# Kernel tuning notes

Measured on AMD Instinct MI355X. Metric: run time of the kernel, lower is better.

The kernel has to match this reference:

```python
import jax, jax.numpy as jnp
import numpy as np

N = 8192        # nodes (A.shape[0])
D_IN = 128      # input_dim
D_OUT = 128     # output_dim
D_THETA = 256   # hardcoded in GCN_liner_theta_1
DROP_KEEP = 0.8 # DropEdge percent


def setup_inputs() -> dict:
    key = jax.random.key(0)
    ks = jax.random.split(key, 6)
    H = jax.random.normal(ks[0], (N, D_IN), dtype=jnp.float32)
    U = jax.random.uniform(ks[1], (N, N), dtype=jnp.float32)
    upper = jnp.triu((U < 0.01).astype(jnp.float32), 1)
    A_adj = upper + upper.T + jnp.eye(N, dtype=jnp.float32)
    bn_gamma = jnp.ones((D_IN,), jnp.float32)
    bn_beta = jnp.zeros((D_IN,), jnp.float32)
    W_theta = jax.random.normal(ks[2], (D_THETA, D_IN), jnp.float32) * 0.05
    b_theta = jnp.zeros((D_THETA,), jnp.float32)
    W_out = jax.random.normal(ks[3], (D_OUT, D_IN), jnp.float32) * 0.05
    b_out = jnp.zeros((D_OUT,), jnp.float32)
    return {"H": H, "A_adj": A_adj, "bn_gamma": bn_gamma, "bn_beta": bn_beta,
            "W_theta": W_theta, "b_theta": b_theta, "W_out": W_out, "b_out": b_out}


def reference(H, A_adj, bn_gamma, bn_beta, W_theta, b_theta, W_out, b_out):
    n = H.shape[0]
    # BatchNorm1d in training mode: batch stats over the node dimension
    mean = H.mean(axis=0)
    var = H.var(axis=0)  # biased, matches torch training normalization
    Hn = (H - mean) * jax.lax.rsqrt(var + 1e-5) * bn_gamma + bn_beta

    # theta projection -> pairwise euclidean distances
    Hx = Hn @ W_theta.T + b_theta                     # [N, 256]
    sq = jnp.sum(Hx * Hx, axis=1)                     # [N]
    dist = sq[:, None] + sq[None, :] - 2.0 * (Hx @ Hx.T)
    dist = jnp.sqrt(jnp.clip(dist, 1e-12, None))      # [N, N]

    A = jnp.exp(-0.2 * dist)
    A = jnp.clip(jax.nn.sigmoid(A), 0.1, None)
    # DropEdge detaches A in the original (A never carries grad)
    A = jax.lax.stop_gradient(A)

    dkey = jax.random.key(42)
    keep = jax.random.uniform(dkey, (n, n)) < DROP_KEEP
    triu = jnp.triu(jnp.ones((n, n), dtype=bool), 0)
    Bt = jnp.where(triu & keep, A, 0.0)
    B = Bt + Bt.T - jnp.diag(jnp.diag(Bt))

    mask = jnp.ceil(A_adj * 1e-5)
    A2 = B * mask + jnp.eye(n, dtype=B.dtype)
    A3 = jnp.where(A2 > 0.6, A2, 0.0)                 # threshold (host loop in torch)

    # symmetric normalization D^-1/2 A D^-1/2 without dense diag matmuls
    d_inv_sqrt = jax.lax.rsqrt(A3.sum(axis=1))        # diag always >= 1
    A_hat = A3 * d_inv_sqrt[:, None] * d_inv_sqrt[None, :]

    out = A_hat @ (Hn @ W_out.T + b_out)              # [N, D_OUT]
    out = jnp.where(out >= 0, out, 0.01 * out)        # LeakyReLU(0.01)
    return out, A3
```

## Files before the change

### kernel.cpp

```cpp
#include <hip/hip_runtime.h>
#include <cstdint>
#include <cstddef>

#define N 8192
#define DIN 128
#define DTH 256
#define DOUT 128
#define ROWCAP 256
#define LISTCAP 256

typedef float vfloat4 __attribute__((ext_vector_type(4)));

__device__ __forceinline__ void threefry_0_42(uint32_t x0, uint32_t x1,
                                              uint32_t& o0, uint32_t& o1) {
  const uint32_t ks0 = 0u;
  const uint32_t ks1 = 42u;
  const uint32_t ks2 = 0x1BD11BDAu ^ 0u ^ 42u;
  x0 += ks0; x1 += ks1;
#define TF_R(r) { x0 += x1; x1 = (x1 << (r)) | (x1 >> (32 - (r))); x1 ^= x0; }
  TF_R(13) TF_R(15) TF_R(26) TF_R(6)
  x0 += ks1; x1 += ks2 + 1u;
  TF_R(17) TF_R(29) TF_R(16) TF_R(24)
  x0 += ks2; x1 += ks0 + 2u;
  TF_R(13) TF_R(15) TF_R(26) TF_R(6)
  x0 += ks0; x1 += ks1 + 3u;
  TF_R(17) TF_R(29) TF_R(16) TF_R(24)
  x0 += ks1; x1 += ks2 + 4u;
  TF_R(13) TF_R(15) TF_R(26) TF_R(6)
  x0 += ks2; x1 += ks0 + 5u;
#undef TF_R
  o0 = x0; o1 = x1;
}

__device__ __forceinline__ bool dropedge_keep(uint32_t t) {
  uint32_t y0, y1;
  threefry_0_42(0u, t, y0, y1);
  uint32_t bits = y0 ^ y1;
  float u = __uint_as_float((bits >> 9) | 0x3f800000u) - 1.0f;
  return u < 0.8f;
}

__device__ __forceinline__ unsigned short f2bf(float v) {
  uint32_t u = __float_as_uint(v);
  u += 0x7fffu + ((u >> 16) & 1u);
  return (unsigned short)(u >> 16);
}

__global__ __launch_bounds__(256) void k_pre(
    const float* __restrict__ H,
    const float* __restrict__ Wt, const float* __restrict__ bt,
    const float* __restrict__ Wo, const float* __restrict__ bo,
    float* __restrict__ part_s, float* __restrict__ part_s2,
    float* __restrict__ Wc, float* __restrict__ bc,
    float* __restrict__ deg ) {
  int b = blockIdx.x;
  int tid = threadIdx.x;
  if (b < 64) {
    __shared__ float ls[8][DIN];
    __shared__ float ls2[8][DIN];
    int rg = tid >> 5;
    int c4 = tid & 31;
    int rbase = b * 128;
    float s[4] = {0,0,0,0}, s2[4] = {0,0,0,0};
    for (int k = 0; k < 16; ++k) {
      int r = rbase + rg + k * 8;
      float4 h = ((const float4*)(H + (size_t)r * DIN))[c4];
      s[0] += h.x; s2[0] += h.x * h.x;
      s[1] += h.y; s2[1] += h.y * h.y;
      s[2] += h.z; s2[2] += h.z * h.z;
      s[3] += h.w; s2[3] += h.w * h.w;
    }
#pragma unroll
    for (int q = 0; q < 4; ++q) { ls[rg][c4*4+q] = s[q]; ls2[rg][c4*4+q] = s2[q]; }
    __syncthreads();
    if (tid < DIN) {
      float a = 0.f, bb = 0.f;
#pragma unroll
      for (int g = 0; g < 8; ++g) { a += ls[g][tid]; bb += ls2[g][tid]; }
      part_s[b * DIN + tid] = a;
      part_s2[b * DIN + tid] = bb;
    }
  } else if (b < 256) {
    int idx = (b - 64) * 256 + tid;
    int k = idx / 384, c = idx % 384;
    Wc[idx] = (c < 256) ? Wt[(size_t)c * DIN + k] : Wo[(size_t)(c - 256) * DIN + k];
  } else if (b < 258) {
    int c = (b - 256) * 256 + tid;
    if (c < 384) bc[c] = (c < 256) ? bt[c] : bo[c - 256];
  } else {
    int g = (b - 258) * 256 + tid;
    ((int4*)deg)[g] = make_int4(0, 0, 0, 0);
  }
}

__global__ __launch_bounds__(256) void k_rows(
    const float* __restrict__ H,
    const float* __restrict__ part_s, const float* __restrict__ part_s2,
    const float* __restrict__ gamma, const float* __restrict__ beta,
    const float* __restrict__ Wc, const float* __restrict__ bc,
    unsigned short* __restrict__ Hxh, float* __restrict__ HW,
    float* __restrict__ sq, float* __restrict__ A3) {
  int tid = threadIdx.x;
  int b = blockIdx.x;
  if (b >= 512) {
    vfloat4* row = (vfloat4*)(A3 + (size_t)(b - 512) * N);
    const vfloat4 z = {0.f, 0.f, 0.f, 0.f};
#pragma unroll
    for (int it = 0; it < 8; ++it)
      __builtin_nontemporal_store(z, row + tid + it * 256);
    return;
  }
  __shared__ __align__(16) float ssc[DIN];
  __shared__ __align__(16) float ssh[DIN];
  __shared__ float hn[16][DIN];
  if (tid < DIN) {
    float s = 0.f, s2 = 0.f;
    for (int g = 0; g < 64; ++g) { s += part_s[g*DIN+tid]; s2 += part_s2[g*DIN+tid]; }
    float mean = s * (1.0f / N);
    float var  = s2 * (1.0f / N) - mean * mean;
    float sc = rsqrtf(var + 1e-5f) * gamma[tid];
    ssc[tid] = sc;
    ssh[tid] = beta[tid] - mean * sc;
  }
  __syncthreads();
  int base = b * 16;
#pragma unroll
  for (int k = 0; k < 2; ++k) {
    int f = tid + k * 256;
    int r = f >> 5, c4 = f & 31;
    float4 h  = ((const float4*)(H + (size_t)(base + r) * DIN))[c4];
    float4 sc = ((const float4*)ssc)[c4];
    float4 sh = ((const float4*)ssh)[c4];
    h.x = h.x * sc.x + sh.x; h.y = h.y * sc.y + sh.y;
    h.z = h.z * sc.z + sh.z; h.w = h.w * sc.w + sh.w;
    ((float4*)hn[r])[c4] = h;
  }
  __syncthreads();
  int w = tid >> 6, lane = tid & 63;
  int r0 = w * 4;
  float acc[4][6];
#pragma unroll
  for (int r = 0; r < 4; ++r)
#pragma unroll
    for (int q = 0; q < 6; ++q) acc[r][q] = 0.f;

  for (int k4 = 0; k4 < 32; ++k4) {
    float4 h[4];
#pragma unroll
    for (int r = 0; r < 4; ++r) h[r] = ((const float4*)hn[r0 + r])[k4];
#pragma unroll
    for (int kk = 0; kk < 4; ++kk) {
      const float* wrow = Wc + (size_t)(k4 * 4 + kk) * 384 + lane;
      float wv[6];
#pragma unroll
      for (int q = 0; q < 6; ++q) wv[q] = wrow[64 * q];
#pragma unroll
      for (int r = 0; r < 4; ++r) {
        float hs = (kk == 0) ? h[r].x : (kk == 1) ? h[r].y
                 : (kk == 2) ? h[r].z : h[r].w;
#pragma unroll
        for (int q = 0; q < 6; ++q) acc[r][q] += hs * wv[q];
      }
    }
  }
#pragma unroll
  for (int r = 0; r < 4; ++r) {
    int row = base + r0 + r;
    float s = 0.f;
#pragma unroll
    for (int q = 0; q < 4; ++q) {
      float v = acc[r][q] + bc[lane + 64 * q];
      Hxh[(size_t)row * DTH + lane + 64 * q] = f2bf(v);
      s += v * v;
    }
#pragma unroll
    for (int off = 32; off > 0; off >>= 1) s += __shfl_xor(s, off, 64);
    if (lane == 0) sq[row] = s;
#pragma unroll
    for (int q = 4; q < 6; ++q) {
      float v = acc[r][q] + bc[lane + 64 * q];
      HW[(size_t)row * DOUT + lane + 64 * (q - 4)] = v;
    }
  }
}

__global__ __launch_bounds__(256) void k_main(
    const float* __restrict__ A_adj, const unsigned short* __restrict__ Hxh,
    const float* __restrict__ sq, float* __restrict__ A3,
    float* __restrict__ deg, int* __restrict__ nnz_cnt,
    int* __restrict__ nnz_idx, float* __restrict__ nnz_val) {
  int i = blockIdx.x;
  int tid = threadIdx.x;
  __shared__ float4 hx4[64];
  __shared__ int   s_list[LISTCAP];
  __shared__ int   s_cnt;
  if (tid == 0) s_cnt = 0;
  ((float*)hx4)[tid] = __uint_as_float(((uint32_t)Hxh[(size_t)i * DTH + tid]) << 16);
  __syncthreads();

  const vfloat4* arow = (const vfloat4*)(A_adj + (size_t)i * N);
  int q0 = i >> 2;
  for (int q4 = q0 + tid; q4 < N / 4; q4 += 256) {
    vfloat4 a = __builtin_nontemporal_load(arow + q4);
    int jb = q4 * 4;
    float av[4] = {a.x, a.y, a.z, a.w};
#pragma unroll
    for (int q = 0; q < 4; ++q) {
      int j = jb + q;
      if (av[q] != 0.f && j >= i) {
        int p = atomicAdd(&s_cnt, 1);
        if (p < LISTCAP) s_list[p] = j;
      }
    }
  }
  __syncthreads();

  int M = min(s_cnt, LISTCAP);
  float sqi = sq[i];
  for (int t = tid; t < M; t += 256) {
    int j = s_list[t];
    bool keep = dropedge_keep((uint32_t)i * (uint32_t)N + (uint32_t)j);
    float dist;
    if (j == i) {
      dist = 1e-6f;
    } else {
      const uint4* hj = (const uint4*)(Hxh + (size_t)j * DTH);
      float dot = 0.f;
#pragma unroll 8
      for (int c = 0; c < 32; ++c) {
        uint4 u = hj[c];
        float4 f0 = hx4[2 * c], f1 = hx4[2 * c + 1];
        dot += __uint_as_float(u.x << 16) * f0.x
             + __uint_as_float(u.x & 0xffff0000u) * f0.y
             + __uint_as_float(u.y << 16) * f0.z
             + __uint_as_float(u.y & 0xffff0000u) * f0.w
             + __uint_as_float(u.z << 16) * f1.x
             + __uint_as_float(u.z & 0xffff0000u) * f1.y
             + __uint_as_float(u.w << 16) * f1.z
             + __uint_as_float(u.w & 0xffff0000u) * f1.w;
      }
      dist = sqrtf(fmaxf(sqi + sq[j] - 2.0f * dot, 1e-12f));
    }
    float aval = expf(-0.2f * dist);
    float sg = fmaxf(1.0f / (1.0f + expf(-aval)), 0.1f);
    float bb = keep ? sg : 0.0f;
    float a2 = bb + ((i == j) ? 1.0f : 0.0f);
    float a3v = (a2 > 0.6f) ? a2 : 0.0f;
    if (a3v != 0.f) {
      A3[(size_t)i * N + j] = a3v;
      atomicAdd(&deg[i], a3v);
      int p = atomicAdd(&nnz_cnt[i], 1);
      if (p < ROWCAP) {
        nnz_idx[(size_t)i * ROWCAP + p] = j;
        nnz_val[(size_t)i * ROWCAP + p] = a3v;
      }
      if (j != i) {
        A3[(size_t)j * N + i] = a3v;
        atomicAdd(&deg[j], a3v);
        int p2 = atomicAdd(&nnz_cnt[j], 1);
        if (p2 < ROWCAP) {
          nnz_idx[(size_t)j * ROWCAP + p2] = i;
          nnz_val[(size_t)j * ROWCAP + p2] = a3v;
        }
      }
    }
  }
}

__global__ __launch_bounds__(128) void k_post(
    const float* __restrict__ HW, const float* __restrict__ deg,
    const int* __restrict__ nnz_cnt, const int* __restrict__ nnz_idx,
    const float* __restrict__ nnz_val, float* __restrict__ out) {
  int i = blockIdx.x;
  int c = threadIdx.x;
  int cnt = min(nnz_cnt[i], ROWCAP);
  float acc = 0.f;
  for (int e = 0; e < cnt; ++e) {
    int j = nnz_idx[(size_t)i * ROWCAP + e];
    float v = nnz_val[(size_t)i * ROWCAP + e];
    acc += v * rsqrtf(deg[j]) * HW[(size_t)j * DOUT + c];
  }
  float o = rsqrtf(deg[i]) * acc;
  out[(size_t)i * DOUT + c] = (o >= 0.f) ? o : 0.01f * o;
}

extern "C" void kernel_launch(void* const* d_in, const int* in_sizes, int n_in,
                              void* d_out, int out_size, void* d_ws, size_t ws_size,
                              hipStream_t stream) {
  const float* H     = (const float*)d_in[0];
  const float* A_adj = (const float*)d_in[1];
  const float* gamma = (const float*)d_in[2];
  const float* beta  = (const float*)d_in[3];
  const float* Wt    = (const float*)d_in[4];
  const float* bt    = (const float*)d_in[5];
  const float* Wo    = (const float*)d_in[6];
  const float* bo    = (const float*)d_in[7];

  float* out = (float*)d_out;
  float* A3  = out + (size_t)N * DOUT;

  float* ws    = (float*)d_ws;
  unsigned short* Hxh = (unsigned short*)ws;
  float* sq    = ws + (size_t)N * 128;
  float* HW    = sq + N;
  float* deg   = HW + (size_t)N * DOUT;
  int*   nnz_cnt = (int*)(deg + N);
  int*   nnz_idx = nnz_cnt + N;
  float* nnz_val = (float*)(nnz_idx + (size_t)N * ROWCAP);
  float* part_s  = nnz_val + (size_t)N * ROWCAP;
  float* part_s2 = part_s + 64 * DIN;
  float* Wc      = part_s2 + 64 * DIN;
  float* bc      = Wc + 128 * 384;

  k_pre<<<274, 256, 0, stream>>>(H, Wt, bt, Wo, bo, part_s, part_s2, Wc, bc, deg);
  k_rows<<<512 + N, 256, 0, stream>>>(H, part_s, part_s2, gamma, beta, Wc, bc,
                                      Hxh, HW, sq, A3);
  k_main<<<N, 256, 0, stream>>>(A_adj, Hxh, sq, A3, deg, nnz_cnt, nnz_idx, nnz_val);
  k_post<<<N, DOUT, 0, stream>>>(HW, deg, nnz_cnt, nnz_idx, nnz_val, out);
}
```

Measured before the change: 461.4 us.

## Move adjacency scan into row-projection kernel and shrink edge kernel to one wavefront

The scan of the dense adjacency matrix that builds each row's upper-triangular edge list moves out of the edge kernel. It now runs in the same launch as the row projection and A3 zeroing, on extra blocks, and writes a compact 16-bit edge index list and count per row to workspace. The edge kernel then reads these lists and runs with 64 threads per row instead of 256. The aim is to overlap the bandwidth-bound adjacency read with the projection's compute and zero-fill, and to stop the low-parallelism edge work from occupying wide blocks. The cost is an extra global round-trip for the edge lists, and the 16-bit indices rely on N fitting in unsigned short.

Result: slower. 473.9 us (+2.7%).

```diff
diff --git a/kernel.cpp b/kernel.cpp
--- a/kernel.cpp
+++ b/kernel.cpp
@@ -93,21 +93,52 @@
   }
 }
 
-__global__ __launch_bounds__(256) void k_rows(
+__global__ __launch_bounds__(256) void k_mid(
     const float* __restrict__ H,
     const float* __restrict__ part_s, const float* __restrict__ part_s2,
     const float* __restrict__ gamma, const float* __restrict__ beta,
     const float* __restrict__ Wc, const float* __restrict__ bc,
+    const float* __restrict__ A_adj,
     unsigned short* __restrict__ Hxh, float* __restrict__ HW,
-    float* __restrict__ sq, float* __restrict__ A3) {
+    float* __restrict__ sq, float* __restrict__ A3,
+    unsigned short* __restrict__ edge_idx, int* __restrict__ edge_cnt) {
   int tid = threadIdx.x;
   int b = blockIdx.x;
   if (b >= 512) {
-    vfloat4* row = (vfloat4*)(A3 + (size_t)(b - 512) * N);
-    const vfloat4 z = {0.f, 0.f, 0.f, 0.f};
-#pragma unroll
-    for (int it = 0; it < 8; ++it)
-      __builtin_nontemporal_store(z, row + tid + it * 256);
+    int t = b - 512;
+    int row = t >> 1;
+    if ((t & 1) == 0) {
+      vfloat4* rp = (vfloat4*)(A3 + (size_t)row * N);
+      const vfloat4 z = {0.f, 0.f, 0.f, 0.f};
+#pragma unroll
+      for (int it = 0; it < 8; ++it)
+        __builtin_nontemporal_store(z, rp + tid + it * 256);
+    } else {
+      __shared__ unsigned short s_list[LISTCAP];
+      __shared__ int s_cnt;
+      if (tid == 0) s_cnt = 0;
+      __syncthreads();
+      const vfloat4* arow = (const vfloat4*)(A_adj + (size_t)row * N);
+      int q0 = row >> 2;
+      for (int q4 = q0 + tid; q4 < N / 4; q4 += 256) {
+        vfloat4 a = __builtin_nontemporal_load(arow + q4);
+        int jb = q4 * 4;
+        float av[4] = {a.x, a.y, a.z, a.w};
+#pragma unroll
+        for (int q = 0; q < 4; ++q) {
+          int j = jb + q;
+          if (av[q] != 0.f && j >= row) {
+            int p = atomicAdd(&s_cnt, 1);
+            if (p < LISTCAP) s_list[p] = (unsigned short)j;
+          }
+        }
+      }
+      __syncthreads();
+      int M = min(s_cnt, LISTCAP);
+      for (int t2 = tid; t2 < M; t2 += 256)
+        edge_idx[(size_t)row * LISTCAP + t2] = s_list[t2];
+      if (tid == 0) edge_cnt[row] = M;
+    }
     return;
   }
   __shared__ __align__(16) float ssc[DIN];
@@ -184,41 +215,21 @@
   }
 }
 
-__global__ __launch_bounds__(256) void k_main(
-    const float* __restrict__ A_adj, const unsigned short* __restrict__ Hxh,
-    const float* __restrict__ sq, float* __restrict__ A3,
-    float* __restrict__ deg, int* __restrict__ nnz_cnt,
+__global__ __launch_bounds__(64) void k_edges(
+    const unsigned short* __restrict__ Hxh, const float* __restrict__ sq,
+    const unsigned short* __restrict__ edge_idx, const int* __restrict__ edge_cnt,
+    float* __restrict__ A3, float* __restrict__ deg, int* __restrict__ nnz_cnt,
     int* __restrict__ nnz_idx, float* __restrict__ nnz_val) {
   int i = blockIdx.x;
   int tid = threadIdx.x;
   __shared__ float4 hx4[64];
-  __shared__ int   s_list[LISTCAP];
-  __shared__ int   s_cnt;
-  if (tid == 0) s_cnt = 0;
-  ((float*)hx4)[tid] = __uint_as_float(((uint32_t)Hxh[(size_t)i * DTH + tid]) << 16);
+  for (int t = tid; t < DTH; t += 64)
+    ((float*)hx4)[t] = __uint_as_float(((uint32_t)Hxh[(size_t)i * DTH + t]) << 16);
   __syncthreads();
-
-  const vfloat4* arow = (const vfloat4*)(A_adj + (size_t)i * N);
-  int q0 = i >> 2;
-  for (int q4 = q0 + tid; q4 < N / 4; q4 += 256) {
-    vfloat4 a = __builtin_nontemporal_load(arow + q4);
-    int jb = q4 * 4;
-    float av[4] = {a.x, a.y, a.z, a.w};
-#pragma unroll
-    for (int q = 0; q < 4; ++q) {
-      int j = jb + q;
-      if (av[q] != 0.f && j >= i) {
-        int p = atomicAdd(&s_cnt, 1);
-        if (p < LISTCAP) s_list[p] = j;
-      }
-    }
-  }
-  __syncthreads();
-
-  int M = min(s_cnt, LISTCAP);
+  int cnt = edge_cnt[i];
   float sqi = sq[i];
-  for (int t = tid; t < M; t += 256) {
-    int j = s_list[t];
+  for (int t = tid; t < cnt; t += 64) {
+    int j = edge_idx[(size_t)i * LISTCAP + t];
     bool keep = dropedge_keep((uint32_t)i * (uint32_t)N + (uint32_t)j);
     float dist;
     if (j == i) {
@@ -311,10 +322,13 @@
   float* part_s2 = part_s + 64 * DIN;
   float* Wc      = part_s2 + 64 * DIN;
   float* bc      = Wc + 128 * 384;
+  int*   edge_cnt = (int*)(bc + 384);
+  unsigned short* edge_idx = (unsigned short*)(edge_cnt + N);
 
   k_pre<<<274, 256, 0, stream>>>(H, Wt, bt, Wo, bo, part_s, part_s2, Wc, bc, deg);
-  k_rows<<<512 + N, 256, 0, stream>>>(H, part_s, part_s2, gamma, beta, Wc, bc,
-                                      Hxh, HW, sq, A3);
-  k_main<<<N, 256, 0, stream>>>(A_adj, Hxh, sq, A3, deg, nnz_cnt, nnz_idx, nnz_val);
+  k_mid<<<512 + 2 * N, 256, 0, stream>>>(H, part_s, part_s2, gamma, beta, Wc, bc,
+                                         A_adj, Hxh, HW, sq, A3, edge_idx, edge_cnt);
+  k_edges<<<N, 64, 0, stream>>>(Hxh, sq, edge_idx, edge_cnt, A3, deg,
+                                nnz_cnt, nnz_idx, nnz_val);
   k_post<<<N, DOUT, 0, stream>>>(HW, deg, nnz_cnt, nnz_idx, nnz_val, out);
 }
```

## Process full adjacency rows per block, writing dense A3 rows and degrees without atomics

Applied to the files above, without the earlier changes.

The main kernel now scans each whole adjacency row instead of only the upper triangle. It computes every edge value itself, so the symmetric scatter to row j is no longer needed. Each block writes its full A3 row (zeros included) with nontemporal stores, which removes the separate zero-fill pass, and it reduces the degree in-block, which removes the global atomics and the deg clear. The cost is that each pairwise dot product and threefry draw is now done twice, and every thread holds 8 float4 loads in registers.

Measured after the change: 1.163 ms. 2.52x slower.

```diff
diff --git a/kernel.cpp b/kernel.cpp
--- a/kernel.cpp
+++ b/kernel.cpp
@@ -7,7 +7,6 @@
 #define DTH 256
 #define DOUT 128
 #define ROWCAP 256
-#define LISTCAP 256
 
 typedef float vfloat4 __attribute__((ext_vector_type(4)));
 
@@ -51,8 +50,7 @@
     const float* __restrict__ Wt, const float* __restrict__ bt,
     const float* __restrict__ Wo, const float* __restrict__ bo,
     float* __restrict__ part_s, float* __restrict__ part_s2,
-    float* __restrict__ Wc, float* __restrict__ bc,
-    float* __restrict__ deg ) {
+    float* __restrict__ Wc, float* __restrict__ bc) {
   int b = blockIdx.x;
   int tid = threadIdx.x;
   if (b < 64) {
@@ -84,12 +82,9 @@
     int idx = (b - 64) * 256 + tid;
     int k = idx / 384, c = idx % 384;
     Wc[idx] = (c < 256) ? Wt[(size_t)c * DIN + k] : Wo[(size_t)(c - 256) * DIN + k];
-  } else if (b < 258) {
+  } else {
     int c = (b - 256) * 256 + tid;
     if (c < 384) bc[c] = (c < 256) ? bt[c] : bo[c - 256];
-  } else {
-    int g = (b - 258) * 256 + tid;
-    ((int4*)deg)[g] = make_int4(0, 0, 0, 0);
   }
 }
 
@@ -99,17 +94,9 @@
     const float* __restrict__ gamma, const float* __restrict__ beta,
     const float* __restrict__ Wc, const float* __restrict__ bc,
     unsigned short* __restrict__ Hxh, float* __restrict__ HW,
-    float* __restrict__ sq, float* __restrict__ A3) {
+    float* __restrict__ sq) {
   int tid = threadIdx.x;
   int b = blockIdx.x;
-  if (b >= 512) {
-    vfloat4* row = (vfloat4*)(A3 + (size_t)(b - 512) * N);
-    const vfloat4 z = {0.f, 0.f, 0.f, 0.f};
-#pragma unroll
-    for (int it = 0; it < 8; ++it)
-      __builtin_nontemporal_store(z, row + tid + it * 256);
-    return;
-  }
   __shared__ __align__(16) float ssc[DIN];
   __shared__ __align__(16) float ssh[DIN];
   __shared__ float hn[16][DIN];
@@ -184,7 +171,7 @@
   }
 }
 
-__global__ __launch_bounds__(256) void k_main(
+__global__ __launch_bounds__(256) void k_scan(
     const float* __restrict__ A_adj, const unsigned short* __restrict__ Hxh,
     const float* __restrict__ sq, float* __restrict__ A3,
     float* __restrict__ deg, int* __restrict__ nnz_cnt,
@@ -192,78 +179,83 @@
   int i = blockIdx.x;
   int tid = threadIdx.x;
   __shared__ float4 hx4[64];
-  __shared__ int   s_list[LISTCAP];
-  __shared__ int   s_cnt;
+  __shared__ float s_deg[4];
+  __shared__ int s_cnt;
+  __shared__ unsigned short s_j[ROWCAP];
+  __shared__ float s_v[ROWCAP];
   if (tid == 0) s_cnt = 0;
   ((float*)hx4)[tid] = __uint_as_float(((uint32_t)Hxh[(size_t)i * DTH + tid]) << 16);
   __syncthreads();
 
   const vfloat4* arow = (const vfloat4*)(A_adj + (size_t)i * N);
-  int q0 = i >> 2;
-  for (int q4 = q0 + tid; q4 < N / 4; q4 += 256) {
-    vfloat4 a = __builtin_nontemporal_load(arow + q4);
-    int jb = q4 * 4;
-    float av[4] = {a.x, a.y, a.z, a.w};
+  vfloat4 a[8];
+#pragma unroll
+  for (int it = 0; it < 8; ++it)
+    a[it] = __builtin_nontemporal_load(arow + tid + it * 256);
+
+  float sqi = sq[i];
+  float dsum = 0.f;
+  vfloat4* orow = (vfloat4*)(A3 + (size_t)i * N);
+#pragma unroll
+  for (int it = 0; it < 8; ++it) {
+    float av[4] = {a[it].x, a[it].y, a[it].z, a[it].w};
+    float ov[4] = {0.f, 0.f, 0.f, 0.f};
+    int jb = (tid + it * 256) * 4;
 #pragma unroll
     for (int q = 0; q < 4; ++q) {
-      int j = jb + q;
-      if (av[q] != 0.f && j >= i) {
-        int p = atomicAdd(&s_cnt, 1);
-        if (p < LISTCAP) s_list[p] = j;
-      }
-    }
-  }
-  __syncthreads();
-
-  int M = min(s_cnt, LISTCAP);
-  float sqi = sq[i];
-  for (int t = tid; t < M; t += 256) {
-    int j = s_list[t];
-    bool keep = dropedge_keep((uint32_t)i * (uint32_t)N + (uint32_t)j);
-    float dist;
-    if (j == i) {
-      dist = 1e-6f;
-    } else {
-      const uint4* hj = (const uint4*)(Hxh + (size_t)j * DTH);
-      float dot = 0.f;
+      if (av[q] != 0.f) {
+        int j = jb + q;
+        uint32_t r = (uint32_t)min(i, j), c = (uint32_t)max(i, j);
+        bool keep = dropedge_keep(r * (uint32_t)N + c);
+        float dist;
+        if (j == i) {
+          dist = 1e-6f;
+        } else {
+          const uint4* hj = (const uint4*)(Hxh + (size_t)j * DTH);
+          float dot = 0.f;
 #pragma unroll 8
-      for (int c = 0; c < 32; ++c) {
-        uint4 u = hj[c];
-        float4 f0 = hx4[2 * c], f1 = hx4[2 * c + 1];
-        dot += __uint_as_float(u.x << 16) * f0.x
-             + __uint_as_float(u.x & 0xffff0000u) * f0.y
-             + __uint_as_float(u.y << 16) * f0.z
-             + __uint_as_float(u.y & 0xffff0000u) * f0.w
-             + __uint_as_float(u.z << 16) * f1.x
-             + __uint_as_float(u.z & 0xffff0000u) * f1.y
-             + __uint_as_float(u.w << 16) * f1.z
-             + __uint_as_float(u.w & 0xffff0000u) * f1.w;
-      }
-      dist = sqrtf(fmaxf(sqi + sq[j] - 2.0f * dot, 1e-12f));
-    }
-    float aval = expf(-0.2f * dist);
-    float sg = fmaxf(1.0f / (1.0f + expf(-aval)), 0.1f);
-    float bb = keep ? sg : 0.0f;
-    float a2 = bb + ((i == j) ? 1.0f : 0.0f);
-    float a3v = (a2 > 0.6f) ? a2 : 0.0f;
-    if (a3v != 0.f) {
-      A3[(size_t)i * N + j] = a3v;
-      atomicAdd(&deg[i], a3v);
-      int p = atomicAdd(&nnz_cnt[i], 1);
-      if (p < ROWCAP) {
-        nnz_idx[(size_t)i * ROWCAP + p] = j;
-        nnz_val[(size_t)i * ROWCAP + p] = a3v;
-      }
-      if (j != i) {
-        A3[(size_t)j * N + i] = a3v;
-        atomicAdd(&deg[j], a3v);
-        int p2 = atomicAdd(&nnz_cnt[j], 1);
-        if (p2 < ROWCAP) {
-          nnz_idx[(size_t)j * ROWCAP + p2] = i;
-          nnz_val[(size_t)j * ROWCAP + p2] = a3v;
+          for (int cc = 0; cc < 32; ++cc) {
+            uint4 u = hj[cc];
+            float4 f0 = hx4[2 * cc], f1 = hx4[2 * cc + 1];
+            dot += __uint_as_float(u.x << 16) * f0.x
+                 + __uint_as_float(u.x & 0xffff0000u) * f0.y
+                 + __uint_as_float(u.y << 16) * f0.z
+                 + __uint_as_float(u.y & 0xffff0000u) * f0.w
+                 + __uint_as_float(u.z << 16) * f1.x
+                 + __uint_as_float(u.z & 0xffff0000u) * f1.y
+                 + __uint_as_float(u.w << 16) * f1.z
+                 + __uint_as_float(u.w & 0xffff0000u) * f1.w;
+          }
+          dist = sqrtf(fmaxf(sqi + sq[j] - 2.0f * dot, 1e-12f));
+        }
+        float aval = expf(-0.2f * dist);
+        float sg = fmaxf(1.0f / (1.0f + expf(-aval)), 0.1f);
+        float bb = keep ? sg : 0.0f;
+        float a2 = bb + ((j == i) ? 1.0f : 0.0f);
+        float a3v = (a2 > 0.6f) ? a2 : 0.0f;
+        if (a3v != 0.f) {
+          ov[q] = a3v;
+          dsum += a3v;
+          int p = atomicAdd(&s_cnt, 1);
+          if (p < ROWCAP) { s_j[p] = (unsigned short)j; s_v[p] = a3v; }
         }
       }
     }
+    vfloat4 o = {ov[0], ov[1], ov[2], ov[3]};
+    __builtin_nontemporal_store(o, orow + tid + it * 256);
+  }
+#pragma unroll
+  for (int off = 32; off > 0; off >>= 1) dsum += __shfl_xor(dsum, off, 64);
+  if ((tid & 63) == 0) s_deg[tid >> 6] = dsum;
+  __syncthreads();
+  if (tid == 0) {
+    deg[i] = s_deg[0] + s_deg[1] + s_deg[2] + s_deg[3];
+    nnz_cnt[i] = min(s_cnt, ROWCAP);
+  }
+  int M = min(s_cnt, ROWCAP);
+  for (int t = tid; t < M; t += 256) {
+    nnz_idx[(size_t)i * ROWCAP + t] = s_j[t];
+    nnz_val[(size_t)i * ROWCAP + t] = s_v[t];
   }
 }
 
@@ -312,9 +304,9 @@
   float* Wc      = part_s2 + 64 * DIN;
   float* bc      = Wc + 128 * 384;
 
-  k_pre<<<274, 256, 0, stream>>>(H, Wt, bt, Wo, bo, part_s, part_s2, Wc, bc, deg);
-  k_rows<<<512 + N, 256, 0, stream>>>(H, part_s, part_s2, gamma, beta, Wc, bc,
-                                      Hxh, HW, sq, A3);
-  k_main<<<N, 256, 0, stream>>>(A_adj, Hxh, sq, A3, deg, nnz_cnt, nnz_idx, nnz_val);
+  k_pre<<<258, 256, 0, stream>>>(H, Wt, bt, Wo, bo, part_s, part_s2, Wc, bc);
+  k_rows<<<N / 16, 256, 0, stream>>>(H, part_s, part_s2, gamma, beta, Wc, bc,
+                                     Hxh, HW, sq);
+  k_scan<<<N, 256, 0, stream>>>(A_adj, Hxh, sq, A3, deg, nnz_cnt, nnz_idx, nnz_val);
   k_post<<<N, DOUT, 0, stream>>>(HW, deg, nnz_cnt, nnz_idx, nnz_val, out);
 }
```
